# Optimization experiments

Measured on AMD Instinct MI355X. Metric: run time of the kernel, lower is better.

The kernel has to match this reference:

```python
import jax, jax.numpy as jnp
import numpy as np

N_NODES = 100000


def setup_inputs() -> dict:
    key = jax.random.key(0)
    ks = jax.random.split(key, 6)
    x = jax.random.normal(ks[0], (N_NODES, 3), dtype=jnp.float32)
    edge_index = jax.random.randint(ks[1], (2, 1600000), 0, N_NODES, dtype=jnp.int32)
    W1 = jax.random.normal(ks[2], (6, 64), dtype=jnp.float32) * 0.2
    b1 = jnp.zeros((64,), dtype=jnp.float32)
    W2 = jax.random.normal(ks[3], (67, 128), dtype=jnp.float32) * 0.1
    b2 = jnp.zeros((128,), dtype=jnp.float32)
    Wc = jax.random.normal(ks[4], (128, 5), dtype=jnp.float32) * 0.1
    bc = jnp.zeros((5,), dtype=jnp.float32)
    return {"x": x, "edge_index": edge_index, "W1": W1, "b1": b1,
            "W2": W2, "b2": b2, "Wc": Wc, "bc": bc}


def _pointnet_conv(h, rel, src, dst, W, b, n):
    # gather neighbor features, MLP on [h_j, pos_j - pos_i], max-aggregate per node
    msg = jnp.concatenate([h[src], rel], axis=-1) @ W + b  # [E, out]
    agg = jax.ops.segment_max(msg, dst, num_segments=n)    # [N, out]
    return jax.nn.relu(agg)  # relu also maps -inf (isolated nodes) to 0


def reference(x, edge_index, W1, b1, W2, b2, Wc, bc):
    src, dst = edge_index[0], edge_index[1]
    pos = x  # forward uses data.x for both x and pos
    rel = pos[src] - pos[dst]                       # [E, 3]
    h = _pointnet_conv(x, rel, src, dst, W1, b1, N_NODES)   # [N, 64]
    h = _pointnet_conv(h, rel, src, dst, W2, b2, N_NODES)   # [N, 128]
    logits = h @ Wc + bc                            # [N, 5]
    return jax.nn.log_softmax(logits, axis=-1)
```

## Files before the change

kernel.cpp:

```cpp
#include <hip/hip_runtime.h>
#include <cstdint>

#define CAP 56
#define NBITS 8
#define BINSZ 256
#define BIN_CAP 5120
#define TILE_E 8192
#define SCANN 512

typedef _Float16 h2 __attribute__((ext_vector_type(2)));
typedef _Float16 h4 __attribute__((ext_vector_type(4)));
typedef _Float16 h8 __attribute__((ext_vector_type(8)));

static __device__ inline h8 pkmax8(h8 a, h8 b) {
#if __has_builtin(__builtin_elementwise_max)
    return __builtin_elementwise_max(a, b);
#else
    h8 r;
    #pragma unroll
    for (int i = 0; i < 8; i += 2) {
        h2 aa = { a[i], a[i+1] }, bb = { b[i], b[i+1] }, rr;
        asm("v_pk_max_f16 %0, %1, %2" : "=v"(rr) : "v"(aa), "v"(bb));
        r[i] = rr.x; r[i+1] = rr.y;
    }
    return r;
#endif
}

__global__ __launch_bounds__(256) void bin_kernel(
    const int* __restrict__ ei, int* __restrict__ bin_cnt,
    int* __restrict__ pairs, int E, int nbins)
{
    __shared__ int hist[SCANN];
    __shared__ int sc[SCANN];
    __shared__ int gbase[SCANN];
    __shared__ int lofs[SCANN];
    __shared__ int words[TILE_E];
    __shared__ unsigned short binOf[TILE_E];
    int t = threadIdx.x;
    for (int i = t; i < SCANN; i += 256) { hist[i] = 0; lofs[i] = 0; }
    __syncthreads();
    int e0 = blockIdx.x * TILE_E;
    int s[32], d[32];
    #pragma unroll
    for (int i = 0; i < 32; ++i) {
        int e = e0 + t + i * 256;
        bool ok = e < E;
        s[i] = ok ? ei[e] : 0;
        d[i] = ok ? ei[E + e] : -1;
        if (ok) atomicAdd(&hist[d[i] >> NBITS], 1);
    }
    __syncthreads();
    sc[t] = hist[t]; sc[t + 256] = hist[t + 256];
    __syncthreads();
    for (int off = 1; off < SCANN; off <<= 1) {
        int i0 = t, i1 = t + 256;
        int v0 = (i0 >= off) ? sc[i0 - off] : 0;
        int v1 = (i1 >= off) ? sc[i1 - off] : 0;
        __syncthreads();
        sc[i0] += v0; sc[i1] += v1;
        __syncthreads();
    }
    for (int i = t; i < nbins; i += 256)
        gbase[i] = atomicAdd(&bin_cnt[i], hist[i]);
    __syncthreads();
    #pragma unroll
    for (int i = 0; i < 32; ++i) {
        if (d[i] >= 0) {
            int b = d[i] >> NBITS;
            int p = atomicAdd(&lofs[b], 1);
            int slot = (sc[b] - hist[b]) + p;
            words[slot] = s[i] | ((d[i] & (BINSZ - 1)) << 17);
            binOf[slot] = (unsigned short)b;
        }
    }
    __syncthreads();
    int total = sc[nbins - 1];
    for (int i = t; i < total; i += 256) {
        int b = binOf[i];
        int off = gbase[b] + (i - (sc[b] - hist[b]));
        if (off < BIN_CAP) pairs[b * BIN_CAP + off] = words[i];
    }
}

__global__ __launch_bounds__(256) void scatter2_kernel(
    const int* __restrict__ pairs, const int* __restrict__ bin_cnt,
    int* __restrict__ cursor, int* __restrict__ bucket, int N)
{
    __shared__ int cur[BINSZ];
    __shared__ int lbuck[BINSZ * CAP];
    int t = threadIdx.x;
    int b = blockIdx.x;
    for (int i = t; i < BINSZ; i += 256) cur[i] = 0;
    __syncthreads();
    int cnt = min(bin_cnt[b], BIN_CAP);
    const int* pp = pairs + b * BIN_CAP;
    for (int i = t; i < cnt; i += 256) {
        int w = pp[i];
        int p = atomicAdd(&cur[w >> 17], 1);
        if (p < CAP) lbuck[(w >> 17) * CAP + p] = w & 0x1FFFF;
    }
    __syncthreads();
    int nbase = b * BINSZ;
    for (int dl = t; dl < BINSZ; dl += 256) {
        int n = nbase + dl;
        if (n >= N) continue;
        int c = min(cur[dl], CAP);
        int e = (c + 7) & ~7;
        int s0 = (c > 0) ? lbuck[dl * CAP] : 0;
        for (int p = c; p < e; ++p) lbuck[dl * CAP + p] = s0;
        cursor[n] = c;
    }
    __syncthreads();
    int4* dst = (int4*)(bucket + (size_t)nbase * CAP);
    const int4* srcv = (const int4*)lbuck;
    for (int i = t; i < BINSZ * CAP / 4; i += 256) dst[i] = srcv[i];
}

__global__ __launch_bounds__(256) void xpack_kernel(
    const float* __restrict__ x, float4* __restrict__ xp,
    int* __restrict__ bin_cnt, int N)
{
    int n = blockIdx.x * 256 + threadIdx.x;
    if (n < N) xp[n] = make_float4(x[n*3], x[n*3+1], x[n*3+2], 0.f);
    if (blockIdx.x == 0) {
        bin_cnt[threadIdx.x] = 0;
        bin_cnt[threadIdx.x + 256] = 0;
    }
}

__global__ __launch_bounds__(256) void agg1_gemm_kernel(
    const float4* __restrict__ xp, const int* __restrict__ cursor,
    const int* __restrict__ bucket, const float* __restrict__ W1,
    const float* __restrict__ b1, const float* __restrict__ W2,
    const float* __restrict__ b2, h4* __restrict__ u2h, int N)
{
    __shared__ float h1T[64][72];
    int tid = threadIdx.x;
    int n0  = blockIdx.x * 64;
    int sub = tid & 15;
    int ng  = tid >> 4;

    float4 q0 = ((const float4*)(W1 + 0*64))[sub];
    float4 q1 = ((const float4*)(W1 + 1*64))[sub];
    float4 q2 = ((const float4*)(W1 + 2*64))[sub];
    float4 t0 = ((const float4*)(W1 + 3*64))[sub];
    float4 t1 = ((const float4*)(W1 + 4*64))[sub];
    float4 t2 = ((const float4*)(W1 + 5*64))[sub];
    float4 c0 = make_float4(q0.x+t0.x, q0.y+t0.y, q0.z+t0.z, q0.w+t0.w);
    float4 c1 = make_float4(q1.x+t1.x, q1.y+t1.y, q1.z+t1.z, q1.w+t1.w);
    float4 c2 = make_float4(q2.x+t2.x, q2.y+t2.y, q2.z+t2.z, q2.w+t2.w);
    float4 bb = ((const float4*)b1)[sub];

    #pragma unroll
    for (int pass = 0; pass < 4; ++pass) {
        int nl = pass * 16 + ng;
        int n  = n0 + nl;
        float4 m = make_float4(-3e38f, -3e38f, -3e38f, -3e38f);
        int cnt = 0;
        if (n < N) {
            cnt = cursor[n];
            int rounds = (cnt + 7) & ~7;
            const int4* brow4 = (const int4*)(bucket + (size_t)n * CAP);
            int4 ia = brow4[0], ib = brow4[1];
            for (int j0 = 0; j0 < rounds; j0 += 8) {
                int4 na = brow4[(j0 >> 2) + 2];
                int4 nb = brow4[(j0 >> 2) + 3];
                float4 xs[8];
                xs[0] = xp[ia.x]; xs[1] = xp[ia.y]; xs[2] = xp[ia.z]; xs[3] = xp[ia.w];
                xs[4] = xp[ib.x]; xs[5] = xp[ib.y]; xs[6] = xp[ib.z]; xs[7] = xp[ib.w];
                #pragma unroll
                for (int u = 0; u < 8; ++u) {
                    float4 v;
                    v.x = fmaf(xs[u].x, c0.x, fmaf(xs[u].y, c1.x, xs[u].z * c2.x));
                    v.y = fmaf(xs[u].x, c0.y, fmaf(xs[u].y, c1.y, xs[u].z * c2.y));
                    v.z = fmaf(xs[u].x, c0.z, fmaf(xs[u].y, c1.z, xs[u].z * c2.z));
                    v.w = fmaf(xs[u].x, c0.w, fmaf(xs[u].y, c1.w, xs[u].z * c2.w));
                    m.x = fmaxf(m.x, v.x); m.y = fmaxf(m.y, v.y);
                    m.z = fmaxf(m.z, v.z); m.w = fmaxf(m.w, v.w);
                }
                ia = na; ib = nb;
            }
        }
        float4 xd = (n < N) ? xp[n] : make_float4(0.f, 0.f, 0.f, 0.f);
        h1T[4*sub+0][nl] = (cnt > 0) ? fmaxf(m.x + bb.x - (xd.x*t0.x + xd.y*t1.x + xd.z*t2.x), 0.f) : 0.f;
        h1T[4*sub+1][nl] = (cnt > 0) ? fmaxf(m.y + bb.y - (xd.x*t0.y + xd.y*t1.y + xd.z*t2.y), 0.f) : 0.f;
        h1T[4*sub+2][nl] = (cnt > 0) ? fmaxf(m.z + bb.z - (xd.x*t0.z + xd.y*t1.z + xd.z*t2.z), 0.f) : 0.f;
        h1T[4*sub+3][nl] = (cnt > 0) ? fmaxf(m.w + bb.w - (xd.x*t0.w + xd.y*t1.w + xd.z*t2.w), 0.f) : 0.f;
    }
    __syncthreads();

    int fi = tid & 31;
    int ni = tid >> 5;
    float acc[8][4];
    #pragma unroll
    for (int r = 0; r < 8; ++r)
        #pragma unroll
        for (int c = 0; c < 4; ++c) acc[r][c] = 0.f;

    const float4* W2v = (const float4*)W2;
    #pragma unroll 4
    for (int k = 0; k < 64; ++k) {
        float4 w  = W2v[k*32 + fi];
        float4 a0 = *(const float4*)&h1T[k][ni*8];
        float4 a1 = *(const float4*)&h1T[k][ni*8+4];
        float hv[8] = {a0.x,a0.y,a0.z,a0.w,a1.x,a1.y,a1.z,a1.w};
        #pragma unroll
        for (int r = 0; r < 8; ++r) {
            acc[r][0] = fmaf(hv[r], w.x, acc[r][0]);
            acc[r][1] = fmaf(hv[r], w.y, acc[r][1]);
            acc[r][2] = fmaf(hv[r], w.z, acc[r][2]);
            acc[r][3] = fmaf(hv[r], w.w, acc[r][3]);
        }
    }
    float4 bb2 = ((const float4*)b2)[fi];
    float4 wa = W2v[64*32 + fi], wb = W2v[65*32 + fi], wc = W2v[66*32 + fi];
    #pragma unroll
    for (int r = 0; r < 8; ++r) {
        int n = n0 + ni*8 + r;
        if (n >= N) break;
        float4 xd = xp[n];
        h4 o4;
        o4.x = (_Float16)(acc[r][0] + bb2.x + xd.x*wa.x + xd.y*wb.x + xd.z*wc.x);
        o4.y = (_Float16)(acc[r][1] + bb2.y + xd.x*wa.y + xd.y*wb.y + xd.z*wc.y);
        o4.z = (_Float16)(acc[r][2] + bb2.z + xd.x*wa.z + xd.y*wb.z + xd.z*wc.z);
        o4.w = (_Float16)(acc[r][3] + bb2.w + xd.x*wa.w + xd.y*wb.w + xd.z*wc.w);
        u2h[(size_t)n * 32 + fi] = o4;
    }
}

__global__ __launch_bounds__(256) void agg2_head_kernel(
    const float* __restrict__ x, const int* __restrict__ cursor,
    const int* __restrict__ bucket, const float* __restrict__ W2,
    const h8* __restrict__ u2v, const float* __restrict__ Wc,
    const float* __restrict__ bc, float* __restrict__ out, int N)
{
    int gid = blockIdx.x * 256 + threadIdx.x;
    int n   = gid >> 4;
    int sub = threadIdx.x & 15;
    if (n >= N) return;
    int cnt = cursor[n];
    int rounds = (cnt + 7) & ~7;
    const int4* brow4 = (const int4*)(bucket + (size_t)n * CAP);
    const _Float16 NEG = (_Float16)(-60000.0f);
    h8 hm = { NEG, NEG, NEG, NEG, NEG, NEG, NEG, NEG };
    int4 ia = brow4[0], ib = brow4[1];
    for (int j0 = 0; j0 < rounds; j0 += 8) {
        int4 na = brow4[(j0 >> 2) + 2];
        int4 nb = brow4[(j0 >> 2) + 3];
        h8 v0 = u2v[(size_t)ia.x * 16 + sub];
        h8 v1 = u2v[(size_t)ia.y * 16 + sub];
        h8 v2 = u2v[(size_t)ia.z * 16 + sub];
        h8 v3 = u2v[(size_t)ia.w * 16 + sub];
        h8 v4 = u2v[(size_t)ib.x * 16 + sub];
        h8 v5 = u2v[(size_t)ib.y * 16 + sub];
        h8 v6 = u2v[(size_t)ib.z * 16 + sub];
        h8 v7 = u2v[(size_t)ib.w * 16 + sub];
        hm = pkmax8(hm, v0); hm = pkmax8(hm, v1);
        hm = pkmax8(hm, v2); hm = pkmax8(hm, v3);
        hm = pkmax8(hm, v4); hm = pkmax8(hm, v5);
        hm = pkmax8(hm, v6); hm = pkmax8(hm, v7);
        ia = na; ib = nb;
    }
    const float4* W2v = (const float4*)W2;
    float4 wa0 = W2v[64*32 + sub*2], wa1 = W2v[64*32 + sub*2 + 1];
    float4 wb0 = W2v[65*32 + sub*2], wb1 = W2v[65*32 + sub*2 + 1];
    float4 wc0 = W2v[66*32 + sub*2], wc1 = W2v[66*32 + sub*2 + 1];
    float x0 = x[n*3], x1 = x[n*3+1], x2 = x[n*3+2];
    float hh[8];
    hh[0] = (cnt > 0) ? fmaxf((float)hm[0] - (x0*wa0.x + x1*wb0.x + x2*wc0.x), 0.f) : 0.f;
    hh[1] = (cnt > 0) ? fmaxf((float)hm[1] - (x0*wa0.y + x1*wb0.y + x2*wc0.y), 0.f) : 0.f;
    hh[2] = (cnt > 0) ? fmaxf((float)hm[2] - (x0*wa0.z + x1*wb0.z + x2*wc0.z), 0.f) : 0.f;
    hh[3] = (cnt > 0) ? fmaxf((float)hm[3] - (x0*wa0.w + x1*wb0.w + x2*wc0.w), 0.f) : 0.f;
    hh[4] = (cnt > 0) ? fmaxf((float)hm[4] - (x0*wa1.x + x1*wb1.x + x2*wc1.x), 0.f) : 0.f;
    hh[5] = (cnt > 0) ? fmaxf((float)hm[5] - (x0*wa1.y + x1*wb1.y + x2*wc1.y), 0.f) : 0.f;
    hh[6] = (cnt > 0) ? fmaxf((float)hm[6] - (x0*wa1.z + x1*wb1.z + x2*wc1.z), 0.f) : 0.f;
    hh[7] = (cnt > 0) ? fmaxf((float)hm[7] - (x0*wa1.w + x1*wb1.w + x2*wc1.w), 0.f) : 0.f;

    int g = sub * 8;
    float l0 = 0.f, l1 = 0.f, l2 = 0.f, l3 = 0.f, l4 = 0.f;
    #pragma unroll
    for (int k = 0; k < 8; ++k) {
        l0 = fmaf(hh[k], Wc[(g+k)*5+0], l0);
        l1 = fmaf(hh[k], Wc[(g+k)*5+1], l1);
        l2 = fmaf(hh[k], Wc[(g+k)*5+2], l2);
        l3 = fmaf(hh[k], Wc[(g+k)*5+3], l3);
        l4 = fmaf(hh[k], Wc[(g+k)*5+4], l4);
    }
    #pragma unroll
    for (int off = 8; off > 0; off >>= 1) {
        l0 += __shfl_xor(l0, off);
        l1 += __shfl_xor(l1, off);
        l2 += __shfl_xor(l2, off);
        l3 += __shfl_xor(l3, off);
        l4 += __shfl_xor(l4, off);
    }
    l0 += bc[0]; l1 += bc[1]; l2 += bc[2]; l3 += bc[3]; l4 += bc[4];
    float mx  = fmaxf(fmaxf(fmaxf(l0, l1), fmaxf(l2, l3)), l4);
    float s   = expf(l0-mx) + expf(l1-mx) + expf(l2-mx) + expf(l3-mx) + expf(l4-mx);
    float lse = mx + logf(s);
    if (sub < 5) {
        float v = (sub == 0) ? l0 : (sub == 1) ? l1 : (sub == 2) ? l2
                : (sub == 3) ? l3 : l4;
        out[n*5 + sub] = v - lse;
    }
}

extern "C" void kernel_launch(void* const* d_in, const int* in_sizes, int n_in,
                              void* d_out, int out_size, void* d_ws, size_t ws_size,
                              hipStream_t stream)
{
    const float* x  = (const float*)d_in[0];
    const int*   ei = (const int*)d_in[1];
    const float* W1 = (const float*)d_in[2];
    const float* b1 = (const float*)d_in[3];
    const float* W2 = (const float*)d_in[4];
    const float* b2 = (const float*)d_in[5];
    const float* Wc = (const float*)d_in[6];
    const float* bc = (const float*)d_in[7];
    float* out = (float*)d_out;

    int N = in_sizes[0] / 3;
    int E = in_sizes[1] / 2;
    int nbins = (N + BINSZ - 1) / BINSZ;

    char* ws = (char*)d_ws;
    h4*     u2h     = (h4*)    (ws);
    float4* xp      = (float4*)(ws + 25600000);
    int*    pairs   = (int*)   (ws + 27200000);
    int*    bucket  = (int*)   (ws + 35250000);
    int*    cursor  = (int*)   (ws + 57700000);
    int*    bin_cnt = (int*)   (ws + 58200000);

    xpack_kernel<<<(N + 255) / 256, 256, 0, stream>>>(x, xp, bin_cnt, N);
    bin_kernel<<<(E + TILE_E - 1) / TILE_E, 256, 0, stream>>>(
        ei, bin_cnt, pairs, E, nbins);
    scatter2_kernel<<<nbins, 256, 0, stream>>>(pairs, bin_cnt, cursor, bucket, N);

    agg1_gemm_kernel<<<(N + 63) / 64, 256, 0, stream>>>(
        xp, cursor, bucket, W1, b1, W2, b2, u2h, N);
    agg2_head_kernel<<<(N * 16 + 255) / 256, 256, 0, stream>>>(
        x, cursor, bucket, W2, (const h8*)u2h, Wc, bc, out, N);
}
```

Baseline: 224.0 us.

## Shrink edge bins to 128 nodes and swizzle h1 shared-memory layout

Halves the destination-bin size (128 nodes per bin, 1024 bins) and shrinks each binning block's edge tile from 8192 to 2048 edges, extending the histogram scan and bin counter reset to the larger bin count. This launches more binning blocks with fewer registers per thread, aiming for better occupancy and smaller per-bin buffers. Separately, the h1 transpose buffer in the first aggregation kernel gets an XOR-style rotating column swizzle to reduce LDS bank conflicts on the scattered writes. Risks include more global atomics on bin counters and the need for the downstream scatter kernel to agree with the new bin size, since that kernel's indexing depends on BINSZ.

```diff
diff --git a/kernel.cpp b/kernel.cpp
--- a/kernel.cpp
+++ b/kernel.cpp
@@ -2,11 +2,11 @@
 #include <cstdint>
 
 #define CAP 56
-#define NBITS 8
-#define BINSZ 256
-#define BIN_CAP 5120
-#define TILE_E 8192
-#define SCANN 512
+#define NBITS 7
+#define BINSZ 128
+#define BIN_CAP 2560
+#define TILE_E 2048
+#define SCANN 1024
 
 typedef _Float16 h2 __attribute__((ext_vector_type(2)));
 typedef _Float16 h4 __attribute__((ext_vector_type(4)));
@@ -41,9 +41,9 @@
     for (int i = t; i < SCANN; i += 256) { hist[i] = 0; lofs[i] = 0; }
     __syncthreads();
     int e0 = blockIdx.x * TILE_E;
-    int s[32], d[32];
-    #pragma unroll
-    for (int i = 0; i < 32; ++i) {
+    int s[8], d[8];
+    #pragma unroll
+    for (int i = 0; i < 8; ++i) {
         int e = e0 + t + i * 256;
         bool ok = e < E;
         s[i] = ok ? ei[e] : 0;
@@ -51,21 +51,25 @@
         if (ok) atomicAdd(&hist[d[i] >> NBITS], 1);
     }
     __syncthreads();
-    sc[t] = hist[t]; sc[t + 256] = hist[t + 256];
+    for (int i = t; i < SCANN; i += 256) sc[i] = hist[i];
     __syncthreads();
     for (int off = 1; off < SCANN; off <<= 1) {
-        int i0 = t, i1 = t + 256;
-        int v0 = (i0 >= off) ? sc[i0 - off] : 0;
-        int v1 = (i1 >= off) ? sc[i1 - off] : 0;
+        int v[4];
+        #pragma unroll
+        for (int j = 0; j < 4; ++j) {
+            int idx = t + j * 256;
+            v[j] = (idx >= off) ? sc[idx - off] : 0;
+        }
         __syncthreads();
-        sc[i0] += v0; sc[i1] += v1;
+        #pragma unroll
+        for (int j = 0; j < 4; ++j) sc[t + j * 256] += v[j];
         __syncthreads();
     }
     for (int i = t; i < nbins; i += 256)
         gbase[i] = atomicAdd(&bin_cnt[i], hist[i]);
     __syncthreads();
     #pragma unroll
-    for (int i = 0; i < 32; ++i) {
+    for (int i = 0; i < 8; ++i) {
         if (d[i] >= 0) {
             int b = d[i] >> NBITS;
             int p = atomicAdd(&lofs[b], 1);
@@ -124,8 +128,8 @@
     int n = blockIdx.x * 256 + threadIdx.x;
     if (n < N) xp[n] = make_float4(x[n*3], x[n*3+1], x[n*3+2], 0.f);
     if (blockIdx.x == 0) {
-        bin_cnt[threadIdx.x] = 0;
-        bin_cnt[threadIdx.x + 256] = 0;
+        #pragma unroll
+        for (int j = 0; j < 4; ++j) bin_cnt[threadIdx.x + j * 256] = 0;
     }
 }
 
@@ -135,7 +139,7 @@
     const float* __restrict__ b1, const float* __restrict__ W2,
     const float* __restrict__ b2, h4* __restrict__ u2h, int N)
 {
-    __shared__ float h1T[64][72];
+    __shared__ float h1s[64 * 72];
     int tid = threadIdx.x;
     int n0  = blockIdx.x * 64;
     int sub = tid & 15;
@@ -183,10 +187,11 @@
             }
         }
         float4 xd = (n < N) ? xp[n] : make_float4(0.f, 0.f, 0.f, 0.f);
-        h1T[4*sub+0][nl] = (cnt > 0) ? fmaxf(m.x + bb.x - (xd.x*t0.x + xd.y*t1.x + xd.z*t2.x), 0.f) : 0.f;
-        h1T[4*sub+1][nl] = (cnt > 0) ? fmaxf(m.y + bb.y - (xd.x*t0.y + xd.y*t1.y + xd.z*t2.y), 0.f) : 0.f;
-        h1T[4*sub+2][nl] = (cnt > 0) ? fmaxf(m.z + bb.z - (xd.x*t0.z + xd.y*t1.z + xd.z*t2.z), 0.f) : 0.f;
-        h1T[4*sub+3][nl] = (cnt > 0) ? fmaxf(m.w + bb.w - (xd.x*t0.w + xd.y*t1.w + xd.z*t2.w), 0.f) : 0.f;
+        int colphys = ((((nl >> 2) + sub) & 15) << 2) | (nl & 3);
+        h1s[(4*sub+0)*72 + colphys] = (cnt > 0) ? fmaxf(m.x + bb.x - (xd.x*t0.x + xd.y*t1.x + xd.z*t2.x), 0.f) : 0.f;
+        h1s[(4*sub+1)*72 + colphys] = (cnt > 0) ? fmaxf(m.y + bb.y - (xd.x*t0.y + xd.y*t1.y + xd.z*t2.y), 0.f) : 0.f;
+        h1s[(4*sub+2)*72 + colphys] = (cnt > 0) ? fmaxf(m.z + bb.z - (xd.x*t0.z + xd.y*t1.z + xd.z*t2.z), 0.f) : 0.f;
+        h1s[(4*sub+3)*72 + colphys] = (cnt > 0) ? fmaxf(m.w + bb.w - (xd.x*t0.w + xd.y*t1.w + xd.z*t2.w), 0.f) : 0.f;
     }
     __syncthreads();
 
@@ -202,8 +207,10 @@
     #pragma unroll 4
     for (int k = 0; k < 64; ++k) {
         float4 w  = W2v[k*32 + fi];
-        float4 a0 = *(const float4*)&h1T[k][ni*8];
-        float4 a1 = *(const float4*)&h1T[k][ni*8+4];
+        int cga = ((2*ni)     + (k >> 2)) & 15;
+        int cgb = ((2*ni + 1) + (k >> 2)) & 15;
+        float4 a0 = *(const float4*)&h1s[k*72 + cga*4];
+        float4 a1 = *(const float4*)&h1s[k*72 + cgb*4];
         float hv[8] = {a0.x,a0.y,a0.z,a0.w,a1.x,a1.y,a1.z,a1.w};
         #pragma unroll
         for (int r = 0; r < 8; ++r) {
```

Result: slower. 232.7 us (+3.9%).

## Compact neighbor buckets into CSR-like layout and swizzle shared h1 tile

Applied to the files above, without the earlier changes.

Replaces the fixed-stride padded bucket array (CAP ints per node) with a compacted layout. Each node's neighbor list is padded only to a multiple of 8 and placed at an offset found by a block-level prefix scan plus a global atomic. Per-node metadata becomes an int2 (start, count), and both aggregation kernels index through it. This cuts the bucket write traffic and the footprint of the index stream read twice. Separately, the shared h1 tile in agg1_gemm uses a rotated column swizzle to reduce LDS bank conflicts. The cost is extra scan and sync work in scatter2, and bin placement now depends on atomic ordering.

```diff
diff --git a/kernel.cpp b/kernel.cpp
--- a/kernel.cpp
+++ b/kernel.cpp
@@ -85,10 +85,13 @@
 
 __global__ __launch_bounds__(256) void scatter2_kernel(
     const int* __restrict__ pairs, const int* __restrict__ bin_cnt,
-    int* __restrict__ cursor, int* __restrict__ bucket, int N)
+    int2* __restrict__ meta, int* __restrict__ bucket,
+    int* __restrict__ gtot, int N)
 {
     __shared__ int cur[BINSZ];
     __shared__ int lbuck[BINSZ * CAP];
+    __shared__ int sc2[BINSZ];
+    __shared__ int sbase;
     int t = threadIdx.x;
     int b = blockIdx.x;
     for (int i = t; i < BINSZ; i += 256) cur[i] = 0;
@@ -101,41 +104,50 @@
         if (p < CAP) lbuck[(w >> 17) * CAP + p] = w & 0x1FFFF;
     }
     __syncthreads();
-    int nbase = b * BINSZ;
-    for (int dl = t; dl < BINSZ; dl += 256) {
-        int n = nbase + dl;
-        if (n >= N) continue;
-        int c = min(cur[dl], CAP);
-        int e = (c + 7) & ~7;
-        int s0 = (c > 0) ? lbuck[dl * CAP] : 0;
-        for (int p = c; p < e; ++p) lbuck[dl * CAP + p] = s0;
-        cursor[n] = c;
-    }
-    __syncthreads();
-    int4* dst = (int4*)(bucket + (size_t)nbase * CAP);
-    const int4* srcv = (const int4*)lbuck;
-    for (int i = t; i < BINSZ * CAP / 4; i += 256) dst[i] = srcv[i];
+    int c  = min(cur[t], CAP);
+    int pc = (c + 7) & ~7;
+    {
+        int s0 = (c > 0) ? lbuck[t * CAP] : 0;
+        for (int p = c; p < pc; ++p) lbuck[t * CAP + p] = s0;
+        sc2[t] = pc;
+    }
+    __syncthreads();
+    for (int off = 1; off < BINSZ; off <<= 1) {
+        int v = (t >= off) ? sc2[t - off] : 0;
+        __syncthreads();
+        sc2[t] += v;
+        __syncthreads();
+    }
+    if (t == BINSZ - 1) sbase = atomicAdd(gtot, sc2[BINSZ - 1]);
+    __syncthreads();
+    int start = sbase + sc2[t] - pc;
+    int n = b * BINSZ + t;
+    if (n < N) meta[n] = make_int2(start, c);
+    int4* dst = (int4*)bucket;
+    const int4* srcv = (const int4*)(lbuck + t * CAP);
+    for (int p = 0; p < (pc >> 2); ++p) dst[(start >> 2) + p] = srcv[p];
 }
 
 __global__ __launch_bounds__(256) void xpack_kernel(
     const float* __restrict__ x, float4* __restrict__ xp,
-    int* __restrict__ bin_cnt, int N)
+    int* __restrict__ bin_cnt, int* __restrict__ gtot, int N)
 {
     int n = blockIdx.x * 256 + threadIdx.x;
     if (n < N) xp[n] = make_float4(x[n*3], x[n*3+1], x[n*3+2], 0.f);
     if (blockIdx.x == 0) {
         bin_cnt[threadIdx.x] = 0;
         bin_cnt[threadIdx.x + 256] = 0;
+        if (threadIdx.x == 0) *gtot = 0;
     }
 }
 
 __global__ __launch_bounds__(256) void agg1_gemm_kernel(
-    const float4* __restrict__ xp, const int* __restrict__ cursor,
+    const float4* __restrict__ xp, const int2* __restrict__ meta,
     const int* __restrict__ bucket, const float* __restrict__ W1,
     const float* __restrict__ b1, const float* __restrict__ W2,
     const float* __restrict__ b2, h4* __restrict__ u2h, int N)
 {
-    __shared__ float h1T[64][72];
+    __shared__ float h1s[64 * 72];
     int tid = threadIdx.x;
     int n0  = blockIdx.x * 64;
     int sub = tid & 15;
@@ -159,9 +171,10 @@
         float4 m = make_float4(-3e38f, -3e38f, -3e38f, -3e38f);
         int cnt = 0;
         if (n < N) {
-            cnt = cursor[n];
+            int2 mt = meta[n];
+            cnt = mt.y;
             int rounds = (cnt + 7) & ~7;
-            const int4* brow4 = (const int4*)(bucket + (size_t)n * CAP);
+            const int4* brow4 = (const int4*)(bucket + mt.x);
             int4 ia = brow4[0], ib = brow4[1];
             for (int j0 = 0; j0 < rounds; j0 += 8) {
                 int4 na = brow4[(j0 >> 2) + 2];
@@ -183,10 +196,11 @@
             }
         }
         float4 xd = (n < N) ? xp[n] : make_float4(0.f, 0.f, 0.f, 0.f);
-        h1T[4*sub+0][nl] = (cnt > 0) ? fmaxf(m.x + bb.x - (xd.x*t0.x + xd.y*t1.x + xd.z*t2.x), 0.f) : 0.f;
-        h1T[4*sub+1][nl] = (cnt > 0) ? fmaxf(m.y + bb.y - (xd.x*t0.y + xd.y*t1.y + xd.z*t2.y), 0.f) : 0.f;
-        h1T[4*sub+2][nl] = (cnt > 0) ? fmaxf(m.z + bb.z - (xd.x*t0.z + xd.y*t1.z + xd.z*t2.z), 0.f) : 0.f;
-        h1T[4*sub+3][nl] = (cnt > 0) ? fmaxf(m.w + bb.w - (xd.x*t0.w + xd.y*t1.w + xd.z*t2.w), 0.f) : 0.f;
+        int colphys = ((((nl >> 2) + sub) & 15) << 2) | (nl & 3);
+        h1s[(4*sub+0)*72 + colphys] = (cnt > 0) ? fmaxf(m.x + bb.x - (xd.x*t0.x + xd.y*t1.x + xd.z*t2.x), 0.f) : 0.f;
+        h1s[(4*sub+1)*72 + colphys] = (cnt > 0) ? fmaxf(m.y + bb.y - (xd.x*t0.y + xd.y*t1.y + xd.z*t2.y), 0.f) : 0.f;
+        h1s[(4*sub+2)*72 + colphys] = (cnt > 0) ? fmaxf(m.z + bb.z - (xd.x*t0.z + xd.y*t1.z + xd.z*t2.z), 0.f) : 0.f;
+        h1s[(4*sub+3)*72 + colphys] = (cnt > 0) ? fmaxf(m.w + bb.w - (xd.x*t0.w + xd.y*t1.w + xd.z*t2.w), 0.f) : 0.f;
     }
     __syncthreads();
 
@@ -202,8 +216,10 @@
     #pragma unroll 4
     for (int k = 0; k < 64; ++k) {
         float4 w  = W2v[k*32 + fi];
-        float4 a0 = *(const float4*)&h1T[k][ni*8];
-        float4 a1 = *(const float4*)&h1T[k][ni*8+4];
+        int cga = ((2*ni)     + (k >> 2)) & 15;
+        int cgb = ((2*ni + 1) + (k >> 2)) & 15;
+        float4 a0 = *(const float4*)&h1s[k*72 + cga*4];
+        float4 a1 = *(const float4*)&h1s[k*72 + cgb*4];
         float hv[8] = {a0.x,a0.y,a0.z,a0.w,a1.x,a1.y,a1.z,a1.w};
         #pragma unroll
         for (int r = 0; r < 8; ++r) {
@@ -230,7 +246,7 @@
 }
 
 __global__ __launch_bounds__(256) void agg2_head_kernel(
-    const float* __restrict__ x, const int* __restrict__ cursor,
+    const float* __restrict__ x, const int2* __restrict__ meta,
     const int* __restrict__ bucket, const float* __restrict__ W2,
     const h8* __restrict__ u2v, const float* __restrict__ Wc,
     const float* __restrict__ bc, float* __restrict__ out, int N)
@@ -239,9 +255,10 @@
     int n   = gid >> 4;
     int sub = threadIdx.x & 15;
     if (n >= N) return;
-    int cnt = cursor[n];
+    int2 mt = meta[n];
+    int cnt = mt.y;
     int rounds = (cnt + 7) & ~7;
-    const int4* brow4 = (const int4*)(bucket + (size_t)n * CAP);
+    const int4* brow4 = (const int4*)(bucket + mt.x);
     const _Float16 NEG = (_Float16)(-60000.0f);
     h8 hm = { NEG, NEG, NEG, NEG, NEG, NEG, NEG, NEG };
     int4 ia = brow4[0], ib = brow4[1];
@@ -329,16 +346,17 @@
     float4* xp      = (float4*)(ws + 25600000);
     int*    pairs   = (int*)   (ws + 27200000);
     int*    bucket  = (int*)   (ws + 35250000);
-    int*    cursor  = (int*)   (ws + 57700000);
-    int*    bin_cnt = (int*)   (ws + 58200000);
-
-    xpack_kernel<<<(N + 255) / 256, 256, 0, stream>>>(x, xp, bin_cnt, N);
+    int2*   meta    = (int2*)  (ws + 45000000);
+    int*    bin_cnt = (int*)   (ws + 45900000);
+    int*    gtot    = (int*)   (ws + 45904096);
+
+    xpack_kernel<<<(N + 255) / 256, 256, 0, stream>>>(x, xp, bin_cnt, gtot, N);
     bin_kernel<<<(E + TILE_E - 1) / TILE_E, 256, 0, stream>>>(
         ei, bin_cnt, pairs, E, nbins);
-    scatter2_kernel<<<nbins, 256, 0, stream>>>(pairs, bin_cnt, cursor, bucket, N);
+    scatter2_kernel<<<nbins, 256, 0, stream>>>(pairs, bin_cnt, meta, bucket, gtot, N);
 
     agg1_gemm_kernel<<<(N + 63) / 64, 256, 0, stream>>>(
-        xp, cursor, bucket, W1, b1, W2, b2, u2h, N);
+        xp, meta, bucket, W1, b1, W2, b2, u2h, N);
     agg2_head_kernel<<<(N * 16 + 255) / 256, 256, 0, stream>>>(
-        x, cursor, bucket, W2, (const h8*)u2h, Wc, bc, out, N);
-}
+        x, meta, bucket, W2, (const h8*)u2h, Wc, bc, out, N);
+}
```

Result: slower. 228.9 us (+2.2%).

## Fold x packing into bin kernel and swizzle h1 shared-memory layout

Applied to the files above, without the earlier changes.

Removes the separate xpack kernel: the float4 packing of x now runs as a grid-stride loop at the start of bin_kernel, and bin_cnt is zeroed with a memset. The h1 tile in agg1_gemm is stored with an XOR-like rotation of column groups by row to cut LDS bank conflicts on the transposed writes. The memset is still a separate stream operation, so launch count may not drop much, and bin_kernel gains extra memory traffic before its histogram work.

```diff
diff --git a/kernel.cpp b/kernel.cpp
--- a/kernel.cpp
+++ b/kernel.cpp
@@ -28,8 +28,9 @@
 }
 
 __global__ __launch_bounds__(256) void bin_kernel(
-    const int* __restrict__ ei, int* __restrict__ bin_cnt,
-    int* __restrict__ pairs, int E, int nbins)
+    const int* __restrict__ ei, const float* __restrict__ x,
+    float4* __restrict__ xp, int* __restrict__ bin_cnt,
+    int* __restrict__ pairs, int E, int N, int nbins)
 {
     __shared__ int hist[SCANN];
     __shared__ int sc[SCANN];
@@ -38,6 +39,9 @@
     __shared__ int words[TILE_E];
     __shared__ unsigned short binOf[TILE_E];
     int t = threadIdx.x;
+    for (int i = blockIdx.x * 256 + t; i < N; i += gridDim.x * 256)
+        xp[i] = make_float4(x[i*3], x[i*3+1], x[i*3+2], 0.f);
+
     for (int i = t; i < SCANN; i += 256) { hist[i] = 0; lofs[i] = 0; }
     __syncthreads();
     int e0 = blockIdx.x * TILE_E;
@@ -117,25 +121,13 @@
     for (int i = t; i < BINSZ * CAP / 4; i += 256) dst[i] = srcv[i];
 }
 
-__global__ __launch_bounds__(256) void xpack_kernel(
-    const float* __restrict__ x, float4* __restrict__ xp,
-    int* __restrict__ bin_cnt, int N)
-{
-    int n = blockIdx.x * 256 + threadIdx.x;
-    if (n < N) xp[n] = make_float4(x[n*3], x[n*3+1], x[n*3+2], 0.f);
-    if (blockIdx.x == 0) {
-        bin_cnt[threadIdx.x] = 0;
-        bin_cnt[threadIdx.x + 256] = 0;
-    }
-}
-
 __global__ __launch_bounds__(256) void agg1_gemm_kernel(
     const float4* __restrict__ xp, const int* __restrict__ cursor,
     const int* __restrict__ bucket, const float* __restrict__ W1,
     const float* __restrict__ b1, const float* __restrict__ W2,
     const float* __restrict__ b2, h4* __restrict__ u2h, int N)
 {
-    __shared__ float h1T[64][72];
+    __shared__ float h1s[64 * 72];
     int tid = threadIdx.x;
     int n0  = blockIdx.x * 64;
     int sub = tid & 15;
@@ -183,10 +175,11 @@
             }
         }
         float4 xd = (n < N) ? xp[n] : make_float4(0.f, 0.f, 0.f, 0.f);
-        h1T[4*sub+0][nl] = (cnt > 0) ? fmaxf(m.x + bb.x - (xd.x*t0.x + xd.y*t1.x + xd.z*t2.x), 0.f) : 0.f;
-        h1T[4*sub+1][nl] = (cnt > 0) ? fmaxf(m.y + bb.y - (xd.x*t0.y + xd.y*t1.y + xd.z*t2.y), 0.f) : 0.f;
-        h1T[4*sub+2][nl] = (cnt > 0) ? fmaxf(m.z + bb.z - (xd.x*t0.z + xd.y*t1.z + xd.z*t2.z), 0.f) : 0.f;
-        h1T[4*sub+3][nl] = (cnt > 0) ? fmaxf(m.w + bb.w - (xd.x*t0.w + xd.y*t1.w + xd.z*t2.w), 0.f) : 0.f;
+        int colphys = ((((nl >> 2) + sub) & 15) << 2) | (nl & 3);
+        h1s[(4*sub+0)*72 + colphys] = (cnt > 0) ? fmaxf(m.x + bb.x - (xd.x*t0.x + xd.y*t1.x + xd.z*t2.x), 0.f) : 0.f;
+        h1s[(4*sub+1)*72 + colphys] = (cnt > 0) ? fmaxf(m.y + bb.y - (xd.x*t0.y + xd.y*t1.y + xd.z*t2.y), 0.f) : 0.f;
+        h1s[(4*sub+2)*72 + colphys] = (cnt > 0) ? fmaxf(m.z + bb.z - (xd.x*t0.z + xd.y*t1.z + xd.z*t2.z), 0.f) : 0.f;
+        h1s[(4*sub+3)*72 + colphys] = (cnt > 0) ? fmaxf(m.w + bb.w - (xd.x*t0.w + xd.y*t1.w + xd.z*t2.w), 0.f) : 0.f;
     }
     __syncthreads();
 
@@ -202,8 +195,10 @@
     #pragma unroll 4
     for (int k = 0; k < 64; ++k) {
         float4 w  = W2v[k*32 + fi];
-        float4 a0 = *(const float4*)&h1T[k][ni*8];
-        float4 a1 = *(const float4*)&h1T[k][ni*8+4];
+        int cga = ((2*ni)     + (k >> 2)) & 15;
+        int cgb = ((2*ni + 1) + (k >> 2)) & 15;
+        float4 a0 = *(const float4*)&h1s[k*72 + cga*4];
+        float4 a1 = *(const float4*)&h1s[k*72 + cgb*4];
         float hv[8] = {a0.x,a0.y,a0.z,a0.w,a1.x,a1.y,a1.z,a1.w};
         #pragma unroll
         for (int r = 0; r < 8; ++r) {
@@ -332,9 +327,9 @@
     int*    cursor  = (int*)   (ws + 57700000);
     int*    bin_cnt = (int*)   (ws + 58200000);
 
-    xpack_kernel<<<(N + 255) / 256, 256, 0, stream>>>(x, xp, bin_cnt, N);
+    (void)hipMemsetAsync(bin_cnt, 0, 2048, stream);
     bin_kernel<<<(E + TILE_E - 1) / TILE_E, 256, 0, stream>>>(
-        ei, bin_cnt, pairs, E, nbins);
+        ei, x, xp, bin_cnt, pairs, E, N, nbins);
     scatter2_kernel<<<nbins, 256, 0, stream>>>(pairs, bin_cnt, cursor, bucket, N);
 
     agg1_gemm_kernel<<<(N + 63) / 64, 256, 0, stream>>>(
```

Measured after the change: 224.7 us. No clear change (+0.3%).
